# Optimization experiments

Measured on AMD Instinct MI355X. Metric: run time of the kernel, lower is better.

The kernel has to match this reference:

```python
import jax, jax.numpy as jnp
import numpy as np

D_MODEL = 1024
N_HEADS = 16
D_HEAD = D_MODEL // N_HEADS
HIDDEN = 4 * D_MODEL
EPS = 1e-5
ROPE_BASE = 10000.0


def layernorm(x, g, b):
    mu = jnp.mean(x, axis=-1, keepdims=True)
    var = jnp.mean((x - mu) ** 2, axis=-1, keepdims=True)
    return (x - mu) * jax.lax.rsqrt(var + EPS) * g + b


def rope(t, pos):
    # t: (B, N, D), pos: (N,) int -> rotary transform over D (half-split pairs)
    half = t.shape[-1] // 2
    inv_freq = 1.0 / (ROPE_BASE ** (jnp.arange(half, dtype=jnp.float32) / half))
    ang = pos.astype(jnp.float32)[:, None] * inv_freq  # (N, half)
    cos, sin = jnp.cos(ang), jnp.sin(ang)
    t1, t2 = t[..., :half], t[..., half:]
    return jnp.concatenate([t1 * cos - t2 * sin, t1 * sin + t2 * cos], axis=-1)


def setup_inputs() -> dict:
    key = jax.random.key(0)
    ks = jax.random.split(key, 12)
    B, N, D, H = 2, 2048, D_MODEL, HIDDEN
    s = 0.02
    return {
        "x": jax.random.normal(ks[0], (B, N, D), jnp.float32),
        "pos": jnp.arange(N, dtype=jnp.int32),
        "Wq": jax.random.normal(ks[1], (D, D), jnp.float32) * s,
        "bq": jnp.zeros((D,), jnp.float32),
        "Wk": jax.random.normal(ks[2], (D, D), jnp.float32) * s,
        "bk": jnp.zeros((D,), jnp.float32),
        "Wv": jax.random.normal(ks[3], (D, D), jnp.float32) * s,
        "bv": jnp.zeros((D,), jnp.float32),
        "Wo": jax.random.normal(ks[4], (D, D), jnp.float32) * s,
        "bo": jnp.zeros((D,), jnp.float32),
        "g1": jnp.ones((D,), jnp.float32),
        "b1": jnp.zeros((D,), jnp.float32),
        "g2": jnp.ones((D,), jnp.float32),
        "b2": jnp.zeros((D,), jnp.float32),
        "W1": jax.random.normal(ks[5], (D, H), jnp.float32) * s,
        "bm1": jnp.zeros((H,), jnp.float32),
        "W2": jax.random.normal(ks[6], (H, D), jnp.float32) * s,
        "bm2": jnp.zeros((D,), jnp.float32),
    }


def reference(x, pos, Wq, bq, Wk, bk, Wv, bv, Wo, bo, g1, b1, g2, b2, W1, bm1, W2, bm2):
    B, N, D = x.shape
    Hh, dh = N_HEADS, D_HEAD

    # --- attention sublayer (pre-norm) ---
    h = layernorm(x, g1, b1)
    q = h @ Wq + bq
    k = h @ Wk + bk
    v = h @ Wv + bv
    q = rope(q, pos)
    k = rope(k, pos)
    # split heads: (B, Hh, N, dh)
    q = q.reshape(B, N, Hh, dh).transpose(0, 2, 1, 3)
    k = k.reshape(B, N, Hh, dh).transpose(0, 2, 1, 3)
    v = v.reshape(B, N, Hh, dh).transpose(0, 2, 1, 3)
    scores = jnp.einsum("bhqd,bhkd->bhqk", q, k) / jnp.sqrt(jnp.float32(dh))
    attn = jax.nn.softmax(scores, axis=-1)
    ctx = jnp.einsum("bhqk,bhkd->bhqd", attn, v)
    ctx = ctx.transpose(0, 2, 1, 3).reshape(B, N, D)
    x = x + ctx @ Wo + bo

    # --- MLP sublayer (pre-norm, exact GELU) ---
    h = layernorm(x, g2, b2)
    h = jax.nn.gelu(h @ W1 + bm1, approximate=False)
    x = x + h @ W2 + bm2
    return x
```

## Files before the change

### kernel.cpp

```cpp
#include <hip/hip_runtime.h>

typedef __bf16 bf16x8 __attribute__((ext_vector_type(8)));
typedef __bf16 bf16x4 __attribute__((ext_vector_type(4)));
typedef float  f32x4  __attribute__((ext_vector_type(4)));

#define D_MODEL 1024
#define SEQ     2048
#define BATCH   2
#define NH      16
#define DH      64
#define HID     4096
#define ROWS    (BATCH*SEQ)

static __device__ __forceinline__ void gl_lds16(const __bf16* g, __bf16* l) {
  __builtin_amdgcn_global_load_lds(
      (const __attribute__((address_space(1))) unsigned int*)g,
      (__attribute__((address_space(3))) unsigned int*)l, 16, 0, 0);
}

__global__ __launch_bounds__(256) void ln_kernel(
    const float* __restrict__ x, const float* __restrict__ g,
    const float* __restrict__ b, __bf16* __restrict__ out)
{
  int row = blockIdx.x;
  const float* xr = x + (size_t)row * D_MODEL;
  int i0 = threadIdx.x * 4;
  f32x4 xv = *(const f32x4*)(xr + i0);
  float s  = xv[0] + xv[1] + xv[2] + xv[3];
  float ss = xv[0]*xv[0] + xv[1]*xv[1] + xv[2]*xv[2] + xv[3]*xv[3];
#pragma unroll
  for (int off = 1; off < 64; off <<= 1) {
    s  += __shfl_xor(s,  off, 64);
    ss += __shfl_xor(ss, off, 64);
  }
  __shared__ float red[8];
  int wave = threadIdx.x >> 6;
  if ((threadIdx.x & 63) == 0) { red[wave] = s; red[4 + wave] = ss; }
  __syncthreads();
  s  = red[0] + red[1] + red[2] + red[3];
  ss = red[4] + red[5] + red[6] + red[7];
  float mu  = s * (1.0f / D_MODEL);
  float var = ss * (1.0f / D_MODEL) - mu * mu;
  float inv = rsqrtf(var + 1e-5f);
  f32x4 gv = *(const f32x4*)(g + i0);
  f32x4 bv = *(const f32x4*)(b + i0);
  bf16x4 ov;
#pragma unroll
  for (int j = 0; j < 4; ++j)
    ov[j] = (__bf16)((xv[j] - mu) * inv * gv[j] + bv[j]);
  *(bf16x4*)(out + (size_t)row * D_MODEL + i0) = ov;
}

__global__ __launch_bounds__(256) void convT_kernel(
    const float* __restrict__ W, __bf16* __restrict__ Wt, int K, int N)
{
  __shared__ float T[32][33];
  int n0 = blockIdx.x * 32, k0 = blockIdx.y * 32;
  int r  = threadIdx.x >> 3;
  int c4 = (threadIdx.x & 7) * 4;
  f32x4 v = *(const f32x4*)(W + (size_t)(k0 + r) * N + n0 + c4);
#pragma unroll
  for (int i = 0; i < 4; ++i) T[r][c4 + i] = v[i];
  __syncthreads();
  bf16x4 o;
#pragma unroll
  for (int i = 0; i < 4; ++i) o[i] = (__bf16)T[c4 + i][r];
  *(bf16x4*)(Wt + (size_t)(n0 + r) * K + k0 + c4) = o;
}

__global__ void biascat_kernel(const float* __restrict__ a,
                               const float* __restrict__ b,
                               const float* __restrict__ c,
                               float* __restrict__ o)
{
  int i = blockIdx.x * 256 + threadIdx.x;
  o[i] = i < 1024 ? a[i] : (i < 2048 ? b[i - 1024] : c[i - 2048]);
}

__global__ __launch_bounds__(512, 2) void gemm256(
    const __bf16* __restrict__ A, const __bf16* __restrict__ Bt,
    const float* __restrict__ bias, const float* __restrict__ resid,
    void* __restrict__ Cv, int M, int N, int K, int act, int c_fp32)
{
  __shared__ __bf16 As[2][256 * 64];
  __shared__ __bf16 Bs[2][256 * 64];
  int tid = threadIdx.x, lane = tid & 63, wv = tid >> 6;
  int quad = lane >> 4, l16 = lane & 15;
  int wr = wv >> 2, wc = wv & 3;
  int gx = M >> 8, gy = N >> 8;
  int nwg = gx * gy;
  int xcd = blockIdx.x & 7;
  int q = nwg >> 3, r8 = nwg & 7;
  int wg = (xcd < r8 ? xcd * (q + 1) : r8 * (q + 1) + (xcd - r8) * q) + (blockIdx.x >> 3);
  int row0 = (wg % gx) << 8;
  int col0 = (wg / gx) << 8;
  int s_r  = lane >> 3;
  int s_src = ((lane & 7) ^ s_r) * 8;
  int sw = l16 & 7;
  int NT = K >> 6;
  f32x4 acc[8][4] = {};

#define G256_STAGE(kt, b)                                                     \
  {                                                                           \
    int k0_ = (kt) * 64;                                                      \
    _Pragma("unroll")                                                         \
    for (int rd = 0; rd < 4; ++rd) {                                          \
      int rrow = rd * 64 + wv * 8 + s_r;                                      \
      gl_lds16(A  + (size_t)(row0 + rrow) * K + k0_ + s_src,                  \
               &As[b][rd * 4096 + wv * 512]);                                 \
      gl_lds16(Bt + (size_t)(col0 + rrow) * K + k0_ + s_src,                  \
               &Bs[b][rd * 4096 + wv * 512]);                                 \
    }                                                                         \
  }

  G256_STAGE(0, 0);
  G256_STAGE(1, 1);

  for (int t = 0; t < NT; ++t) {
    if (t + 1 < NT) asm volatile("s_waitcnt vmcnt(8)" ::: "memory");
    else            asm volatile("s_waitcnt vmcnt(0)" ::: "memory");
    __builtin_amdgcn_s_barrier();
    const __bf16* Ab = &As[t & 1][0];
    const __bf16* Bb = &Bs[t & 1][0];
    __builtin_amdgcn_s_setprio(1);
#pragma unroll
    for (int kk = 0; kk < 2; ++kk) {
      int slot = ((kk * 4 + quad) ^ sw) * 8;
      bf16x8 bfr[4];
#pragma unroll
      for (int j = 0; j < 4; ++j)
        bfr[j] = *(const bf16x8*)(Bb + (wc * 64 + j * 16 + l16) * 64 + slot);
      bf16x8 afr[8];
#pragma unroll
      for (int i = 0; i < 8; ++i)
        afr[i] = *(const bf16x8*)(Ab + (wr * 128 + i * 16 + l16) * 64 + slot);
#pragma unroll
      for (int i = 0; i < 8; ++i)
#pragma unroll
        for (int j = 0; j < 4; ++j)
          acc[i][j] = __builtin_amdgcn_mfma_f32_16x16x32_bf16(afr[i], bfr[j], acc[i][j], 0, 0, 0);
    }
    __builtin_amdgcn_s_setprio(0);
    __builtin_amdgcn_s_barrier();
    if (t + 2 < NT) G256_STAGE(t + 2, t & 1);
  }

#pragma unroll
  for (int i = 0; i < 8; ++i) {
    int grow = row0 + wr * 128 + i * 16 + quad * 4;
#pragma unroll
    for (int j = 0; j < 4; ++j) {
      int gcol = col0 + wc * 64 + j * 16 + l16;
      float bsv = bias[gcol];
#pragma unroll
      for (int r = 0; r < 4; ++r) {
        size_t off = (size_t)(grow + r) * N + gcol;
        float v = acc[i][j][r] + bsv;
        if (act) v = 0.5f * v * (1.0f + erff(v * 0.70710678118654752f));
        if (resid) v += resid[off];
        if (c_fp32) ((float*)Cv)[off] = v;
        else        ((__bf16*)Cv)[off] = (__bf16)v;
      }
    }
  }
}

__global__ __launch_bounds__(256) void gemm128(
    const __bf16* __restrict__ A, const __bf16* __restrict__ Bt,
    const float* __restrict__ bias, const float* __restrict__ resid,
    void* __restrict__ Cv, int M, int N, int K, int act, int c_fp32)
{
  __shared__ __bf16 As[128 * 64];
  __shared__ __bf16 Bs[128 * 64];
  int tid = threadIdx.x, lane = tid & 63, wv = tid >> 6;
  int quad = lane >> 4, l16 = lane & 15;
  int wr = wv >> 1, wc = wv & 1;
  int gx = M >> 7, gy = N >> 7;
  int blk = blockIdx.x;
  int xcd = blk & 7, t = blk >> 3;
  int row0 = (t % gx) * 128;
  int col0 = (xcd * (gy >> 3) + t / gx) * 128;
  int s_r8 = lane >> 3;
  int s_c8 = lane & 7;
  int s_src = (s_c8 ^ s_r8) * 8;
  int sw = l16 & 7;
  f32x4 acc[4][4] = {};

  for (int k0 = 0; k0 < K; k0 += 64) {
#pragma unroll
    for (int p = 0; p < 4; ++p) {
      int r = p * 32 + wv * 8 + s_r8;
      gl_lds16(A  + (size_t)(row0 + r) * K + k0 + s_src, As + p * 2048 + wv * 512);
      gl_lds16(Bt + (size_t)(col0 + r) * K + k0 + s_src, Bs + p * 2048 + wv * 512);
    }
    __syncthreads();
#pragma unroll
    for (int kk = 0; kk < 2; ++kk) {
      int slot = ((kk * 4 + quad) ^ sw) * 8;
      bf16x8 af[4], bf[4];
#pragma unroll
      for (int i = 0; i < 4; ++i) {
        af[i] = *(const bf16x8*)(As + (wr * 64 + i * 16 + l16) * 64 + slot);
        bf[i] = *(const bf16x8*)(Bs + (wc * 64 + i * 16 + l16) * 64 + slot);
      }
#pragma unroll
      for (int i = 0; i < 4; ++i)
#pragma unroll
        for (int j = 0; j < 4; ++j)
          acc[i][j] = __builtin_amdgcn_mfma_f32_16x16x32_bf16(af[i], bf[j], acc[i][j], 0, 0, 0);
    }
    __syncthreads();
  }
#pragma unroll
  for (int i = 0; i < 4; ++i) {
    int grow = row0 + wr * 64 + i * 16 + quad * 4;
#pragma unroll
    for (int j = 0; j < 4; ++j) {
      int gcol = col0 + wc * 64 + j * 16 + l16;
      float bsv = bias[gcol];
#pragma unroll
      for (int r = 0; r < 4; ++r) {
        size_t off = (size_t)(grow + r) * N + gcol;
        float v = acc[i][j][r] + bsv;
        if (act) v = 0.5f * v * (1.0f + erff(v * 0.70710678118654752f));
        if (resid) v += resid[off];
        if (c_fp32) ((float*)Cv)[off] = v;
        else        ((__bf16*)Cv)[off] = (__bf16)v;
      }
    }
  }
}

__global__ __launch_bounds__(256) void gemm64x128(
    const __bf16* __restrict__ A, const __bf16* __restrict__ Bt,
    const float* __restrict__ bias, const float* __restrict__ resid,
    void* __restrict__ Cv, int M, int N, int K, int act, int c_fp32)
{
  __shared__ __bf16 As[64 * 64];
  __shared__ __bf16 Bs[128 * 64];
  int tid = threadIdx.x, lane = tid & 63, wv = tid >> 6;
  int quad = lane >> 4, l16 = lane & 15;
  int wr = wv >> 1, wc = wv & 1;
  int gx = M >> 6, gy = N >> 7;
  int blk = blockIdx.x;
  int xcd = blk & 7, t = blk >> 3;
  int row0 = (t % gx) * 64;
  int col0 = (xcd * (gy >> 3) + t / gx) * 128;
  int s_r8 = lane >> 3;
  int s_c8 = lane & 7;
  int s_src = (s_c8 ^ s_r8) * 8;
  int sw = l16 & 7;
  f32x4 acc[2][4] = {};

  for (int k0 = 0; k0 < K; k0 += 64) {
#pragma unroll
    for (int p = 0; p < 4; ++p) {
      int r = p * 32 + wv * 8 + s_r8;
      if (p < 2)
        gl_lds16(A + (size_t)(row0 + r) * K + k0 + s_src, As + p * 2048 + wv * 512);
      gl_lds16(Bt + (size_t)(col0 + r) * K + k0 + s_src, Bs + p * 2048 + wv * 512);
    }
    __syncthreads();
#pragma unroll
    for (int kk = 0; kk < 2; ++kk) {
      int slot = ((kk * 4 + quad) ^ sw) * 8;
      bf16x8 af[2], bf[4];
#pragma unroll
      for (int i = 0; i < 2; ++i)
        af[i] = *(const bf16x8*)(As + (wr * 32 + i * 16 + l16) * 64 + slot);
#pragma unroll
      for (int j = 0; j < 4; ++j)
        bf[j] = *(const bf16x8*)(Bs + (wc * 64 + j * 16 + l16) * 64 + slot);
#pragma unroll
      for (int i = 0; i < 2; ++i)
#pragma unroll
        for (int j = 0; j < 4; ++j)
          acc[i][j] = __builtin_amdgcn_mfma_f32_16x16x32_bf16(af[i], bf[j], acc[i][j], 0, 0, 0);
    }
    __syncthreads();
  }
#pragma unroll
  for (int i = 0; i < 2; ++i) {
    int grow = row0 + wr * 32 + i * 16 + quad * 4;
#pragma unroll
    for (int j = 0; j < 4; ++j) {
      int gcol = col0 + wc * 64 + j * 16 + l16;
      float bsv = bias[gcol];
#pragma unroll
      for (int r = 0; r < 4; ++r) {
        size_t off = (size_t)(grow + r) * N + gcol;
        float v = acc[i][j][r] + bsv;
        if (act) v = 0.5f * v * (1.0f + erff(v * 0.70710678118654752f));
        if (resid) v += resid[off];
        if (c_fp32) ((float*)Cv)[off] = v;
        else        ((__bf16*)Cv)[off] = (__bf16)v;
      }
    }
  }
}

__global__ __launch_bounds__(256) void rope_repack(
    const __bf16* __restrict__ qkv, const int* __restrict__ pos,
    __bf16* __restrict__ Qh, __bf16* __restrict__ Kh)
{
  int row = blockIdx.x;
  int b = row >> 11, n = row & (SEQ - 1);
  float p = (float)pos[n];
  const __bf16* qr = qkv + (size_t)row * 3072;
#pragma unroll
  for (int t = 0; t < 2; ++t) {
    int i = threadIdx.x + t * 256;
    float fr  = expf(-9.210340371976184f * ((float)i * (1.0f / 512.0f)));
    float ang = p * fr;
    float sn, c;
    sincosf(ang, &sn, &c);
    float q1 = (float)qr[i],        q2 = (float)qr[512 + i];
    float k1 = (float)qr[1024 + i], k2 = (float)qr[1536 + i];
    int h1 = i >> 6, d1 = i & 63;
    int h2 = (i + 512) >> 6;
    size_t o1 = ((size_t)(b * NH + h1) * SEQ + n) * DH + d1;
    size_t o2 = ((size_t)(b * NH + h2) * SEQ + n) * DH + d1;
    Qh[o1] = (__bf16)((q1 * c - q2 * sn) * 0.125f);
    Qh[o2] = (__bf16)((q1 * sn + q2 * c) * 0.125f);
    Kh[o1] = (__bf16)(k1 * c - k2 * sn);
    Kh[o2] = (__bf16)(k1 * sn + k2 * c);
  }
}

__global__ __launch_bounds__(256) void vtrans_kernel(
    const __bf16* __restrict__ Vsrc, int vstride, __bf16* __restrict__ Vt,
    int blocked)
{
  __shared__ __bf16 T[64][72];
  int bh = blockIdx.x;
  int kb = blockIdx.y * 64;
  int b = bh >> 4, h = bh & 15;
  int tid = threadIdx.x;
#pragma unroll
  for (int t = 0; t < 2; ++t) {
    int u = tid + t * 256;
    int r = u >> 3, seg = (u & 7) * 8;
    bf16x8 v = *(const bf16x8*)(Vsrc + (size_t)(b * SEQ + kb + r) * vstride + h * DH + seg);
    *(bf16x8*)(&T[r][seg]) = v;
  }
  __syncthreads();
#pragma unroll
  for (int t = 0; t < 2; ++t) {
    int u = tid + t * 256;
    int d = u >> 3, ks = (u & 7) * 8;
    bf16x8 o;
#pragma unroll
    for (int i = 0; i < 8; ++i) o[i] = T[ks + i][d];
    if (blocked) {
      int key = kb + ks;
      *(bf16x8*)(Vt + (((size_t)bh * (SEQ / 128) + (key >> 7)) * DH + d) * 128 + (key & 127)) = o;
    } else {
      *(bf16x8*)(Vt + ((size_t)bh * DH + d) * SEQ + kb + ks) = o;
    }
  }
}

#define KS 136
__global__ __launch_bounds__(256) void attn_split(
    const __bf16* __restrict__ Qh, const __bf16* __restrict__ Kh,
    const __bf16* __restrict__ Vt, __bf16* __restrict__ pacc,
    float* __restrict__ pml)
{
  __shared__ __bf16 Ks[128 * 64];
  __shared__ __bf16 Vs[64 * 128];
  __shared__ __bf16 Pl[4][16 * KS];
  int tid = threadIdx.x, lane = tid & 63, wave = tid >> 6;
  int quad = lane >> 4, l16 = lane & 15;
  int blk = blockIdx.x;
  int split = blk >> 10;
  int rr = blk & 1023;
  int bh  = ((rr & 7) << 2) | ((rr >> 3) & 3);
  int q64 = rr >> 5;
  int q0 = q64 * 64 + wave * 16;
  const __bf16* qbase = Qh + (size_t)bh * SEQ * DH;
  const __bf16* kbase = Kh + (size_t)bh * SEQ * DH;
  const __bf16* vbase = Vt + (size_t)bh * SEQ * DH;
  const __bf16* qp = qbase + (size_t)(q0 + l16) * DH + quad * 8;
  bf16x8 qf0 = *(const bf16x8*)(qp);
  bf16x8 qf1 = *(const bf16x8*)(qp + 32);
  float lrow[4] = {0.f, 0.f, 0.f, 0.f};
  f32x4 acc[4] = {};
  __bf16* pw = &Pl[wave][0];
  int s_kr = lane >> 3;
  int s_k8 = lane & 7;
  int s_vd = lane >> 4;
  int s_vs = lane & 15;
  int sw8  = l16 & 7;

  int kb0 = split * (SEQ / 2);
  for (int it = 0; it < (SEQ / 2) / 128; ++it) {
    int kb = kb0 + it * 128;
    const __bf16* kt = kbase + (size_t)kb * DH;
    const __bf16* vt = vbase + (size_t)(kb >> 7) * (DH * 128);
    __syncthreads();
#pragma unroll
    for (int p = 0; p < 4; ++p) {
      int key0 = p * 32 + wave * 8;
      int swz  = (key0 >> 3) & 7;
      gl_lds16(kt + (key0 + s_kr) * DH + ((s_k8 ^ swz) * 8), Ks + p * 2048 + wave * 512);
      int d = p * 16 + wave * 4 + s_vd;
      gl_lds16(vt + d * 128 + ((s_vs ^ (d & 15)) * 8), Vs + p * 2048 + wave * 512);
    }
    __syncthreads();
    f32x4 s[8];
#pragma unroll
    for (int j = 0; j < 8; ++j) {
      const __bf16* kr = Ks + (l16 * 8 + j) * 64;
      bf16x8 kf0 = *(const bf16x8*)(kr + (quad ^ sw8) * 8);
      bf16x8 kf1 = *(const bf16x8*)(kr + ((quad ^ sw8) ^ 4) * 8);
      f32x4 z = {};
      z = __builtin_amdgcn_mfma_f32_16x16x32_bf16(qf0, kf0, z, 0, 0, 0);
      s[j] = __builtin_amdgcn_mfma_f32_16x16x32_bf16(qf1, kf1, z, 0, 0, 0);
    }
#pragma unroll
    for (int r = 0; r < 4; ++r) {
      bf16x8 pv;
      float rs = 0.f;
#pragma unroll
      for (int j = 0; j < 8; ++j) {
        float pj = __expf(s[j][r]);
        rs += pj;
        pv[j] = (__bf16)pj;
      }
      lrow[r] += rs;
      *(bf16x8*)(pw + (quad * 4 + r) * KS + l16 * 8) = pv;
    }
#pragma unroll
    for (int kk = 0; kk < 4; ++kk) {
      bf16x8 pf = *(const bf16x8*)(pw + l16 * KS + kk * 32 + quad * 8);
#pragma unroll
      for (int j = 0; j < 4; ++j) {
        int d = j * 16 + l16;
        bf16x8 vf = *(const bf16x8*)(Vs + d * 128 + (((kk * 4 + quad) ^ (d & 15)) * 8));
        acc[j] = __builtin_amdgcn_mfma_f32_16x16x32_bf16(pf, vf, acc[j], 0, 0, 0);
      }
    }
  }
#pragma unroll
  for (int r = 0; r < 4; ++r)
#pragma unroll
    for (int off = 1; off < 16; off <<= 1) lrow[r] += __shfl_xor(lrow[r], off, 64);
#pragma unroll
  for (int r = 0; r < 4; ++r) {
    int brow = wave * 16 + quad * 4 + r;
#pragma unroll
    for (int j = 0; j < 4; ++j)
      pacc[((size_t)blk * 64 + brow) * 64 + j * 16 + l16] = (__bf16)acc[j][r];
    if (l16 == 0) {
      pml[(size_t)blk * 128 + brow]      = 0.f;
      pml[(size_t)blk * 128 + 64 + brow] = lrow[r];
    }
  }
}

__global__ __launch_bounds__(256) void attn_combine(
    const __bf16* __restrict__ pacc, const float* __restrict__ pml,
    __bf16* __restrict__ ctx)
{
  int bq = blockIdx.x;
  int q64 = bq & 31, bh = bq >> 5;
  int b = bh >> 4, h = bh & 15;
  int tid = threadIdx.x;
  int r = tid >> 2;
  int c = (tid & 3) * 16;
  int blk0 = ((q64 * 4 + (bh & 3)) << 3) | (bh >> 2);
  int blk1 = blk0 + 1024;
  float m0 = pml[(size_t)blk0 * 128 + r], l0 = pml[(size_t)blk0 * 128 + 64 + r];
  float m1 = pml[(size_t)blk1 * 128 + r], l1 = pml[(size_t)blk1 * 128 + 64 + r];
  float m = fmaxf(m0, m1);
  float w0 = __expf(m0 - m), w1 = __expf(m1 - m);
  float inv = 1.0f / (w0 * l0 + w1 * l1);
  size_t r0 = ((size_t)blk0 * 64 + r) * 64 + c;
  size_t r1 = ((size_t)blk1 * 64 + r) * 64 + c;
  size_t ob = ((size_t)(b * SEQ) + q64 * 64 + r) * D_MODEL + h * DH + c;
#pragma unroll
  for (int g = 0; g < 2; ++g) {
    bf16x8 a0 = *(const bf16x8*)(pacc + r0 + g * 8);
    bf16x8 a1 = *(const bf16x8*)(pacc + r1 + g * 8);
    bf16x8 o;
#pragma unroll
    for (int i = 0; i < 8; ++i)
      o[i] = (__bf16)((w0 * (float)a0[i] + w1 * (float)a1[i]) * inv);
    *(bf16x8*)(ctx + ob + g * 8) = o;
  }
}

__global__ __launch_bounds__(256) void rope_inplace(
    __bf16* __restrict__ ql, __bf16* __restrict__ kl,
    const int* __restrict__ pos, int stride)
{
  int row = blockIdx.x;
  int n = row & (SEQ - 1);
  float p = (float)pos[n];
  const size_t rbase = (size_t)row * stride;
#pragma unroll
  for (int t = 0; t < 2; ++t) {
    int i = threadIdx.x + t * 256;
    float fr  = expf(-9.210340371976184f * ((float)i * (1.0f / 512.0f)));
    float ang = p * fr;
    float sn, c;
    sincosf(ang, &sn, &c);
    float q1 = (float)ql[rbase + i], q2 = (float)ql[rbase + 512 + i];
    float k1 = (float)kl[rbase + i], k2 = (float)kl[rbase + 512 + i];
    ql[rbase + i]       = (__bf16)(q1 * c - q2 * sn);
    ql[rbase + 512 + i] = (__bf16)(q1 * sn + q2 * c);
    kl[rbase + i]       = (__bf16)(k1 * c - k2 * sn);
    kl[rbase + 512 + i] = (__bf16)(k1 * sn + k2 * c);
  }
}

__global__ __launch_bounds__(256) void attn_kernel(
    const __bf16* __restrict__ Q, const __bf16* __restrict__ K,
    const __bf16* __restrict__ Vt, __bf16* __restrict__ ctx, int qkstride)
{
  __shared__ __bf16 Pl[4][16 * KS];
  int tid = threadIdx.x, lane = tid & 63, wave = tid >> 6;
  int quad = lane >> 4, l16 = lane & 15;
  int blk = blockIdx.x;
  int q64 = blk & 31;
  int bh  = blk >> 5;
  int b = bh >> 4, h = bh & 15;
  int q0 = q64 * 64 + wave * 16;
  const __bf16* qbase = Q + (size_t)b * SEQ * qkstride + h * DH;
  const __bf16* kbase = K + (size_t)b * SEQ * qkstride + h * DH;
  const __bf16* vbase = Vt + (size_t)bh * DH * SEQ;
  const __bf16* qp = qbase + (size_t)(q0 + l16) * qkstride + quad * 8;
  bf16x8 qf0 = *(const bf16x8*)(qp);
  bf16x8 qf1 = *(const bf16x8*)(qp + 32);
  float mrow[4] = {-1e30f, -1e30f, -1e30f, -1e30f};
  float lrow[4] = {0.f, 0.f, 0.f, 0.f};
  f32x4 acc[4] = {};
  __bf16* pw = &Pl[wave][0];

  for (int kb = 0; kb < SEQ; kb += 128) {
    f32x4 s[8];
#pragma unroll
    for (int j = 0; j < 8; ++j) {
      const __bf16* kp = kbase + (size_t)(kb + l16 * 8 + j) * qkstride + quad * 8;
      bf16x8 kf0 = *(const bf16x8*)(kp);
      bf16x8 kf1 = *(const bf16x8*)(kp + 32);
      f32x4 z = {};
      z = __builtin_amdgcn_mfma_f32_16x16x32_bf16(qf0, kf0, z, 0, 0, 0);
      z = __builtin_amdgcn_mfma_f32_16x16x32_bf16(qf1, kf1, z, 0, 0, 0);
#pragma unroll
      for (int r = 0; r < 4; ++r) s[j][r] = z[r] * 0.125f;
    }
#pragma unroll
    for (int r = 0; r < 4; ++r) {
      float mx = s[0][r];
#pragma unroll
      for (int j = 1; j < 8; ++j) mx = fmaxf(mx, s[j][r]);
#pragma unroll
      for (int off = 1; off < 16; off <<= 1) mx = fmaxf(mx, __shfl_xor(mx, off, 64));
      float mn = fmaxf(mrow[r], mx);
      float al = __expf(mrow[r] - mn);
      float p[8], rs = 0.f;
#pragma unroll
      for (int j = 0; j < 8; ++j) { p[j] = __expf(s[j][r] - mn); rs += p[j]; }
#pragma unroll
      for (int off = 1; off < 16; off <<= 1) rs += __shfl_xor(rs, off, 64);
      lrow[r] = lrow[r] * al + rs;
      mrow[r] = mn;
#pragma unroll
      for (int j = 0; j < 4; ++j) acc[j][r] *= al;
      bf16x8 pv;
#pragma unroll
      for (int j = 0; j < 8; ++j) pv[j] = (__bf16)p[j];
      *(bf16x8*)(pw + (quad * 4 + r) * KS + l16 * 8) = pv;
    }
#pragma unroll
    for (int kk = 0; kk < 4; ++kk) {
      bf16x8 pf = *(const bf16x8*)(pw + l16 * KS + kk * 32 + quad * 8);
#pragma unroll
      for (int j = 0; j < 4; ++j) {
        bf16x8 vf = *(const bf16x8*)(vbase + (size_t)(j * 16 + l16) * SEQ + kb + kk * 32 + quad * 8);
        acc[j] = __builtin_amdgcn_mfma_f32_16x16x32_bf16(pf, vf, acc[j], 0, 0, 0);
      }
    }
  }
#pragma unroll
  for (int r = 0; r < 4; ++r) {
    int row = q0 + quad * 4 + r;
    float inv = 1.0f / lrow[r];
    size_t obase = ((size_t)(b * SEQ) + row) * D_MODEL + h * DH;
#pragma unroll
    for (int j = 0; j < 4; ++j)
      ctx[obase + j * 16 + l16] = (__bf16)(acc[j][r] * inv);
  }
}

extern "C" void kernel_launch(void* const* d_in, const int* in_sizes, int n_in,
                              void* d_out, int out_size, void* d_ws, size_t ws_size,
                              hipStream_t stream)
{
  const float* x   = (const float*)d_in[0];
  const int*   pos = (const int*)  d_in[1];
  const float* Wq  = (const float*)d_in[2];
  const float* bq  = (const float*)d_in[3];
  const float* Wk  = (const float*)d_in[4];
  const float* bk  = (const float*)d_in[5];
  const float* Wv  = (const float*)d_in[6];
  const float* bv  = (const float*)d_in[7];
  const float* Wo  = (const float*)d_in[8];
  const float* bo  = (const float*)d_in[9];
  const float* g1  = (const float*)d_in[10];
  const float* b1  = (const float*)d_in[11];
  const float* g2  = (const float*)d_in[12];
  const float* b2  = (const float*)d_in[13];
  const float* W1  = (const float*)d_in[14];
  const float* bm1 = (const float*)d_in[15];
  const float* W2  = (const float*)d_in[16];
  const float* bm2 = (const float*)d_in[17];
  float* out = (float*)d_out;

  const size_t MB = 1024 * 1024;
  char* w = (char*)d_ws;
  dim3 blk(256);
  dim3 blk512(512);
  dim3 gConvD(D_MODEL / 32, D_MODEL / 32);
  dim3 gConv1(HID / 32, D_MODEL / 32);
  dim3 gConv2(D_MODEL / 32, HID / 32);
  dim3 gVt(BATCH * NH, SEQ / 64);

  if (ws_size >= (size_t)96 * MB) {
    __bf16* hln   = (__bf16*)(w + 0 * MB);
    float*  x1    = (float*) (w + 8 * MB);
    __bf16* qkv   = (__bf16*)(w + 24 * MB);
    __bf16* pacc  = (__bf16*)(w + 24 * MB);
    float*  pml   = (float*) (w + 41 * MB);
    __bf16* hmlp  = (__bf16*)(w + 24 * MB);
    __bf16* Qh    = (__bf16*)(w + 48 * MB);
    __bf16* ctx   = (__bf16*)(w + 48 * MB);
    __bf16* Kh    = (__bf16*)(w + 56 * MB);
    __bf16* W2T   = (__bf16*)(w + 56 * MB);
    __bf16* Vt    = (__bf16*)(w + 64 * MB);
    __bf16* W1T   = (__bf16*)(w + 64 * MB);
    __bf16* WqkvT = (__bf16*)(w + 72 * MB);
    __bf16* WoT   = (__bf16*)(w + 78 * MB);
    float*  bqkv  = (float*) (w + 80 * MB);

    convT_kernel<<<gConvD, blk, 0, stream>>>(Wq, WqkvT,               D_MODEL, D_MODEL);
    convT_kernel<<<gConvD, blk, 0, stream>>>(Wk, WqkvT + 1024 * 1024, D_MODEL, D_MODEL);
    convT_kernel<<<gConvD, blk, 0, stream>>>(Wv, WqkvT + 2048 * 1024, D_MODEL, D_MODEL);
    convT_kernel<<<gConvD, blk, 0, stream>>>(Wo, WoT, D_MODEL, D_MODEL);
    biascat_kernel<<<12, blk, 0, stream>>>(bq, bk, bv, bqkv);
    ln_kernel<<<ROWS, blk, 0, stream>>>(x, g1, b1, hln);
    gemm256<<<(ROWS / 256) * (3072 / 256), blk512, 0, stream>>>(hln, WqkvT, bqkv, nullptr, qkv, ROWS, 3072, D_MODEL, 0, 0);
    rope_repack<<<ROWS, blk, 0, stream>>>(qkv, pos, Qh, Kh);
    vtrans_kernel<<<gVt, blk, 0, stream>>>(qkv + 2048, 3072, Vt, 1);
    attn_split<<<BATCH * NH * (SEQ / 64) * 2, blk, 0, stream>>>(Qh, Kh, Vt, pacc, pml);
    attn_combine<<<BATCH * NH * (SEQ / 64), blk, 0, stream>>>(pacc, pml, ctx);
    convT_kernel<<<gConv1, blk, 0, stream>>>(W1, W1T, D_MODEL, HID);
    convT_kernel<<<gConv2, blk, 0, stream>>>(W2, W2T, HID, D_MODEL);
    gemm64x128<<<(ROWS / 64) * (D_MODEL / 128), blk, 0, stream>>>(ctx, WoT, bo, x, x1, ROWS, D_MODEL, D_MODEL, 0, 1);
    ln_kernel<<<ROWS, blk, 0, stream>>>(x1, g2, b2, hln);
    gemm256<<<(ROWS / 256) * (HID / 256), blk512, 0, stream>>>(hln, W1T, bm1, nullptr, hmlp, ROWS, HID, D_MODEL, 1, 0);
    gemm64x128<<<(ROWS / 64) * (D_MODEL / 128), blk, 0, stream>>>(hmlp, W2T, bm2, x1, out, ROWS, D_MODEL, HID, 0, 1);
  } else {
    __bf16* hln  = (__bf16*)(w + 0 * MB);
    __bf16* vlin = (__bf16*)(w + 8 * MB);
    __bf16* WqT  = (__bf16*)(w + 16 * MB);
    __bf16* WkT  = (__bf16*)(w + 18 * MB);
    __bf16* WvT  = (__bf16*)(w + 20 * MB);
    __bf16* ctx  = (__bf16*)(w + 16 * MB);
    __bf16* WoT  = (__bf16*)(w + 8 * MB);
    __bf16* W1T  = (__bf16*)(w + 8 * MB);
    __bf16* W2T  = (__bf16*)(w + 16 * MB);
    __bf16* Vt   = (__bf16*)(w + 24 * MB);
    __bf16* hmlp = (__bf16*)(w + 24 * MB);
    __bf16* qlin = (__bf16*)d_out;
    __bf16* klin = (__bf16*)d_out + (size_t)ROWS * D_MODEL;
    float*  x1   = (float*)d_out;

    convT_kernel<<<gConvD, blk, 0, stream>>>(Wq, WqT, D_MODEL, D_MODEL);
    convT_kernel<<<gConvD, blk, 0, stream>>>(Wk, WkT, D_MODEL, D_MODEL);
    convT_kernel<<<gConvD, blk, 0, stream>>>(Wv, WvT, D_MODEL, D_MODEL);
    ln_kernel<<<ROWS, blk, 0, stream>>>(x, g1, b1, hln);
    int nLin = (ROWS / 64) * (D_MODEL / 128);
    gemm64x128<<<nLin, blk, 0, stream>>>(hln, WqT, bq, nullptr, qlin, ROWS, D_MODEL, D_MODEL, 0, 0);
    gemm64x128<<<nLin, blk, 0, stream>>>(hln, WkT, bk, nullptr, klin, ROWS, D_MODEL, D_MODEL, 0, 0);
    gemm64x128<<<nLin, blk, 0, stream>>>(hln, WvT, bv, nullptr, vlin, ROWS, D_MODEL, D_MODEL, 0, 0);
    rope_inplace<<<ROWS, blk, 0, stream>>>(qlin, klin, pos, D_MODEL);
    vtrans_kernel<<<gVt, blk, 0, stream>>>(vlin, D_MODEL, Vt, 0);
    attn_kernel<<<BATCH * NH * (SEQ / 64), blk, 0, stream>>>(qlin, klin, Vt, ctx, D_MODEL);
    convT_kernel<<<gConvD, blk, 0, stream>>>(Wo, WoT, D_MODEL, D_MODEL);
    gemm64x128<<<nLin, blk, 0, stream>>>(ctx, WoT, bo, x, x1, ROWS, D_MODEL, D_MODEL, 0, 1);
    ln_kernel<<<ROWS, blk, 0, stream>>>(x1, g2, b2, hln);
    convT_kernel<<<gConv1, blk, 0, stream>>>(W1, W1T, D_MODEL, HID);
    convT_kernel<<<gConv2, blk, 0, stream>>>(W2, W2T, HID, D_MODEL);
    const int CH = 1024;
    for (int c = 0; c < ROWS / CH; ++c) {
      const __bf16* a1 = hln + (size_t)c * CH * D_MODEL;
      gemm128<<<(CH / 128) * (HID / 128), blk, 0, stream>>>(a1, W1T, bm1, nullptr, hmlp, CH, HID, D_MODEL, 1, 0);
      gemm64x128<<<(CH / 64) * (D_MODEL / 128), blk, 0, stream>>>(hmlp, W2T, bm2, x1 + (size_t)c * CH * D_MODEL,
                                          out + (size_t)c * CH * D_MODEL, CH, D_MODEL, HID, 0, 1);
    }
  }
}
```

Measured before the change: 432.7 us.

## Double-buffer LDS in 64x128 GEMM with async prefetch two tiles ahead

Gives the 64x128 GEMM kernel two LDS buffers for the A and B tiles and issues global-to-LDS loads two K-tiles ahead. Explicit vmcnt waits and raw barriers replace the full __syncthreads pair, so loads overlap with the MFMA work. It also raises wave priority around the MFMA section. The cost is double the LDS per block, which may lower occupancy, and reliance on a hand-counted vmcnt value for correctness.

```diff
diff --git a/kernel.cpp b/kernel.cpp
--- a/kernel.cpp
+++ b/kernel.cpp
@@ -236,8 +236,8 @@
     const float* __restrict__ bias, const float* __restrict__ resid,
     void* __restrict__ Cv, int M, int N, int K, int act, int c_fp32)
 {
-  __shared__ __bf16 As[64 * 64];
-  __shared__ __bf16 Bs[128 * 64];
+  __shared__ __bf16 As[2][64 * 64];
+  __shared__ __bf16 Bs[2][128 * 64];
   int tid = threadIdx.x, lane = tid & 63, wv = tid >> 6;
   int quad = lane >> 4, l16 = lane & 15;
   int wr = wv >> 1, wc = wv & 1;
@@ -250,35 +250,54 @@
   int s_c8 = lane & 7;
   int s_src = (s_c8 ^ s_r8) * 8;
   int sw = l16 & 7;
+  int NT = K >> 6;
   f32x4 acc[2][4] = {};
 
-  for (int k0 = 0; k0 < K; k0 += 64) {
-#pragma unroll
-    for (int p = 0; p < 4; ++p) {
-      int r = p * 32 + wv * 8 + s_r8;
-      if (p < 2)
-        gl_lds16(A + (size_t)(row0 + r) * K + k0 + s_src, As + p * 2048 + wv * 512);
-      gl_lds16(Bt + (size_t)(col0 + r) * K + k0 + s_src, Bs + p * 2048 + wv * 512);
-    }
-    __syncthreads();
+#define G64_STAGE(kt, b)                                                      \
+  {                                                                           \
+    int k0_ = (kt) * 64;                                                      \
+    _Pragma("unroll")                                                         \
+    for (int p = 0; p < 4; ++p) {                                             \
+      int r = p * 32 + wv * 8 + s_r8;                                         \
+      if (p < 2)                                                              \
+        gl_lds16(A + (size_t)(row0 + r) * K + k0_ + s_src,                    \
+                 &As[b][p * 2048 + wv * 512]);                                \
+      gl_lds16(Bt + (size_t)(col0 + r) * K + k0_ + s_src,                     \
+               &Bs[b][p * 2048 + wv * 512]);                                  \
+    }                                                                         \
+  }
+
+  G64_STAGE(0, 0);
+  G64_STAGE(1, 1);
+
+  for (int tt = 0; tt < NT; ++tt) {
+    if (tt + 1 < NT) asm volatile("s_waitcnt vmcnt(6)" ::: "memory");
+    else             asm volatile("s_waitcnt vmcnt(0)" ::: "memory");
+    __builtin_amdgcn_s_barrier();
+    const __bf16* Ab = &As[tt & 1][0];
+    const __bf16* Bb = &Bs[tt & 1][0];
+    __builtin_amdgcn_s_setprio(1);
 #pragma unroll
     for (int kk = 0; kk < 2; ++kk) {
       int slot = ((kk * 4 + quad) ^ sw) * 8;
       bf16x8 af[2], bf[4];
 #pragma unroll
       for (int i = 0; i < 2; ++i)
-        af[i] = *(const bf16x8*)(As + (wr * 32 + i * 16 + l16) * 64 + slot);
+        af[i] = *(const bf16x8*)(Ab + (wr * 32 + i * 16 + l16) * 64 + slot);
 #pragma unroll
       for (int j = 0; j < 4; ++j)
-        bf[j] = *(const bf16x8*)(Bs + (wc * 64 + j * 16 + l16) * 64 + slot);
+        bf[j] = *(const bf16x8*)(Bb + (wc * 64 + j * 16 + l16) * 64 + slot);
 #pragma unroll
       for (int i = 0; i < 2; ++i)
 #pragma unroll
         for (int j = 0; j < 4; ++j)
           acc[i][j] = __builtin_amdgcn_mfma_f32_16x16x32_bf16(af[i], bf[j], acc[i][j], 0, 0, 0);
     }
-    __syncthreads();
-  }
+    __builtin_amdgcn_s_setprio(0);
+    __builtin_amdgcn_s_barrier();
+    if (tt + 2 < NT) G64_STAGE(tt + 2, tt & 1);
+  }
+
 #pragma unroll
   for (int i = 0; i < 2; ++i) {
     int grow = row0 + wr * 32 + i * 16 + quad * 4;
```

New measurement: 428.2 us, median of 2. No clear change (-1.1%).
